# Optimization experiments

Hardware: AMD Instinct MI355X
Metric: run time of the kernel (lower is better)

Reference implementation:

```python
import jax, jax.numpy as jnp
import numpy as np

V = 32000   # vocab_size
D = 1024    # dim
NH = 16     # n_heads
HD = 64     # head_dim
L = 2       # n_layers
E = 8       # n_experts
K = 2       # n_active_experts
H = 2048    # expert_dim
B = 2
T = 1024
EPS = 1e-6
THETA = 10000.0
STD = 0.02


def rmsnorm(x, w):
    rms = jax.lax.rsqrt(jnp.mean(x * x, axis=-1, keepdims=True) + EPS)
    return x * rms * w


def rope_cos_sin(t_len):
    inv = 1.0 / (THETA ** (jnp.arange(0, HD, 2, dtype=jnp.float32) / HD))
    t = jnp.arange(t_len, dtype=jnp.float32)
    f = jnp.outer(t, inv)  # [T, HD//2]
    return jnp.cos(f), jnp.sin(f)


def apply_rope(x, cos, sin):
    # x: [B, T, NH, HD]; complex rotation on interleaved (even, odd) pairs
    xr = x[..., 0::2]
    xi = x[..., 1::2]
    c = cos[None, :, None, :]
    s = sin[None, :, None, :]
    out_r = xr * c - xi * s
    out_i = xr * s + xi * c
    return jnp.stack([out_r, out_i], axis=-1).reshape(x.shape)


def setup_inputs() -> dict:
    key = jax.random.key(0)
    ks = jax.random.split(key, 13)
    n = lambda k, shp: (jax.random.normal(k, shp, dtype=jnp.float32) * STD)
    return {
        "tokens": jax.random.randint(ks[0], (B, T), 0, V, dtype=jnp.int64)
                   if jax.config.jax_enable_x64 else
                   jax.random.randint(ks[0], (B, T), 0, V, dtype=jnp.int32),
        "emb": n(ks[1], (V, D)),            # tied embedding / output projection
        "attn_norm_w": jnp.ones((L, D), jnp.float32),
        "wq": n(ks[2], (L, D, D)),
        "wk": n(ks[3], (L, D, D)),
        "wv": n(ks[4], (L, D, D)),
        "wo": n(ks[5], (L, D, D)),
        "ffn_norm_w": jnp.ones((L, D), jnp.float32),
        "gate_w": n(ks[6], (L, D, E)),
        "w1": n(ks[7], (L, E, D, H)),
        "w2": n(ks[8], (L, E, H, D)),
        "w3": n(ks[9], (L, E, D, H)),
        "final_norm_w": jnp.ones((D,), jnp.float32),
    }


def reference(tokens, emb, attn_norm_w, wq, wk, wv, wo, ffn_norm_w,
              gate_w, w1, w2, w3, final_norm_w):
    b, t = tokens.shape
    h = emb[tokens]                                     # [B,T,D]
    cos, sin = rope_cos_sin(t)
    mask = jnp.where(jnp.tril(jnp.ones((t, t), bool)), 0.0, -jnp.inf)
    scale = 1.0 / np.sqrt(HD).astype(np.float32)
    aux_total = jnp.float32(0.0)

    for l in range(L):
        x = h
        # --- attention ---
        hn = rmsnorm(x, attn_norm_w[l])
        q = (hn @ wq[l]).reshape(b, t, NH, HD)
        k = (hn @ wk[l]).reshape(b, t, NH, HD)
        v = (hn @ wv[l]).reshape(b, t, NH, HD)
        q = apply_rope(q, cos, sin)
        k = apply_rope(k, cos, sin)
        scores = jnp.einsum('bqhd,bkhd->bhqk', q, k) * scale + mask
        attn = jax.nn.softmax(scores, axis=-1)
        o = jnp.einsum('bhqk,bkhd->bqhd', attn, v).reshape(b, t, D) @ wo[l]
        x = x + o
        # --- MoE ---
        xf = rmsnorm(x, ffn_norm_w[l]).reshape(-1, D)   # [N,D]
        gate_logits = xf @ gate_w[l]                    # [N,E]
        probs = jax.nn.softmax(gate_logits, axis=-1)
        vals, idx = jax.lax.top_k(probs, K)             # [N,K]
        w = vals / (jnp.sum(vals, axis=-1, keepdims=True) + 1e-8)
        oh = jax.nn.one_hot(idx, E, dtype=jnp.float32)  # [N,K,E]
        combine = jnp.sum(oh * w[..., None], axis=1)    # [N,E]
        tokens_per_expert = oh.sum(axis=1).mean(axis=0)
        aux_total = aux_total + E * jnp.sum(tokens_per_expert * probs.mean(axis=0))
        h1 = jnp.einsum('nd,edh->neh', xf, w1[l])
        h3 = jnp.einsum('nd,edh->neh', xf, w3[l])
        eo = jnp.einsum('neh,ehd->ned', jax.nn.silu(h1) * h3, w2[l])
        moe_out = jnp.einsum('ned,ne->nd', eo, combine).reshape(b, t, D)
        h = x + moe_out

    logits = rmsnorm(h, final_norm_w) @ emb.T           # [B,T,V]
    return logits, aux_total
```

## Files before the change

### kernel.cpp

```cpp
#include <hip/hip_runtime.h>
#include <hip/hip_bf16.h>
#include <math.h>

#define D_MODEL 1024
#define NHEADS  16
#define HDIM    64
#define NEXP    8
#define FFH     2048
#define BATCH   2
#define SEQ     1024
#define NTOK    2048
#define VOCAB   32000
#define LDSS    40

typedef __attribute__((ext_vector_type(4))) float f32x4;
typedef __attribute__((ext_vector_type(2))) float f32x2;
typedef __attribute__((ext_vector_type(8))) __bf16 bf16x8;
typedef __attribute__((ext_vector_type(4))) unsigned short u16x4;

__device__ __forceinline__ unsigned short f2bf(float f) {
    union { float f; unsigned u; } v; v.f = f;
    unsigned r = v.u + 0x7FFFu + ((v.u >> 16) & 1u);
    return (unsigned short)(r >> 16);
}
__device__ __forceinline__ float bf2f(unsigned short u) {
    union { unsigned u; float f; } v; v.u = ((unsigned)u) << 16; return v.f;
}
__device__ __forceinline__ void split3(float x, unsigned short& h, unsigned short& m, unsigned short& l) {
    h = f2bf(x);
    float r1 = x - bf2f(h);
    m = f2bf(r1);
    float r2 = r1 - bf2f(m);
    l = f2bf(r2);
}

#define MFMA(a, b, c) __builtin_amdgcn_mfma_f32_16x16x32_bf16((a), (b), (c), 0, 0, 0)

#define PSA ((long)NTOK * D_MODEL)
#define PSW ((long)D_MODEL * D_MODEL)

__global__ __launch_bounds__(256) void rmsnorm_kernel(const float* __restrict__ x,
    const float* __restrict__ wt, unsigned short* __restrict__ out3)
{
    __shared__ float red[4];
    int n = blockIdx.x;
    int c = threadIdx.x << 2;
    f32x4 v = *(const f32x4*)(x + (long)n*D_MODEL + c);
    float ss = v.x*v.x + v.y*v.y + v.z*v.z + v.w*v.w;
    #pragma unroll
    for (int dd = 32; dd; dd >>= 1) ss += __shfl_xor(ss, dd);
    if ((threadIdx.x & 63) == 0) red[threadIdx.x >> 6] = ss;
    __syncthreads();
    float tot = red[0] + red[1] + red[2] + red[3];
    float rms = rsqrtf(tot * (1.f / D_MODEL) + 1e-6f);
    f32x4 wv = *(const f32x4*)(wt + c);
    f32x4 o = v * rms;
    o = o * wv;
    u16x4 hv, mv, lv;
    #pragma unroll
    for (int j = 0; j < 4; j++) { unsigned short h,m,l; split3(o[j],h,m,l); hv[j]=h; mv[j]=m; lv[j]=l; }
    long idx = (long)n*D_MODEL + c;
    *(u16x4*)(out3 + 0*PSA + idx) = hv;
    *(u16x4*)(out3 + 1*PSA + idx) = mv;
    *(u16x4*)(out3 + 2*PSA + idx) = lv;
}

__global__ __launch_bounds__(256) void wsplitT_kernel(
    const float* __restrict__ wqs, const float* __restrict__ wks, const float* __restrict__ wvs,
    unsigned short* __restrict__ oq, unsigned short* __restrict__ ok, unsigned short* __restrict__ ov)
{
    __shared__ float t[64][65];
    int k0 = blockIdx.x*64, n0 = blockIdx.y*64, z = blockIdx.z;
    const float* src = (z==0) ? wqs : (z==1) ? wks : wvs;
    unsigned short* dst = (z==0) ? oq : (z==1) ? ok : ov;
    int tid = threadIdx.x;
    int a = tid & 63, g = tid >> 6;
    #pragma unroll 4
    for (int i = 0; i < 16; i++) {
        int k = g*16 + i;
        t[k][a] = src[(long)(k0+k)*D_MODEL + n0 + a];
    }
    __syncthreads();
    #pragma unroll 4
    for (int i = 0; i < 16; i++) {
        int n = g*16 + i;
        float v = t[a][n];
        unsigned short h,m,l; split3(v,h,m,l);
        long idx = (long)(n0+n)*D_MODEL + k0 + a;
        dst[0*PSW + idx] = h;
        dst[1*PSW + idx] = m;
        dst[2*PSW + idx] = l;
    }
}

__global__ __launch_bounds__(256, 4) void qkv_kernel(
    const unsigned short* __restrict__ A3,
    const unsigned short* __restrict__ Wq3, const unsigned short* __restrict__ Wk3,
    const unsigned short* __restrict__ Wv3,
    float* __restrict__ qf, float* __restrict__ kf, float* __restrict__ vf)
{
    __shared__ __align__(16) unsigned short As[3][64*LDSS];
    __shared__ __align__(16) unsigned short Bs[3][64*LDSS];
    int z = blockIdx.z;
    const unsigned short* B3 = (z==0) ? Wq3 : (z==1) ? Wk3 : Wv3;
    float* out = (z==0) ? qf : (z==1) ? kf : vf;
    int n0 = blockIdx.x*64, m0 = blockIdx.y*64;
    int tid = threadIdx.x, w = tid >> 6, lane = tid & 63;
    int wm = (w >> 1)*32, wn = (w & 1)*32;
    int lr = lane & 15, lg = lane >> 4;
    f32x4 zero = {0.f,0.f,0.f,0.f};
    f32x4 acc[2][2];
    #pragma unroll
    for (int mi = 0; mi < 2; mi++)
        #pragma unroll
        for (int ni = 0; ni < 2; ni++) acc[mi][ni] = zero;
    int rb = tid >> 3, kc = (tid & 7) << 2;

    for (int k0 = 0; k0 < D_MODEL; k0 += 32) {
        #pragma unroll
        for (int p = 0; p < 2; p++) {
            int r = p*32 + rb;
            #pragma unroll
            for (int s = 0; s < 3; s++) {
                *(u16x4*)&As[s][r*LDSS + kc] = *(const u16x4*)(A3 + s*PSA + (long)(m0+r)*D_MODEL + k0 + kc);
                *(u16x4*)&Bs[s][r*LDSS + kc] = *(const u16x4*)(B3 + s*PSW + (long)(n0+r)*D_MODEL + k0 + kc);
            }
        }
        __syncthreads();
        bf16x8 bf[3][2];
        #pragma unroll
        for (int s = 0; s < 3; s++)
            #pragma unroll
            for (int ni = 0; ni < 2; ni++)
                bf[s][ni] = *(const bf16x8*)&Bs[s][(wn + ni*16 + lr)*LDSS + lg*8];
        #pragma unroll
        for (int mi = 0; mi < 2; mi++) {
            bf16x8 ah = *(const bf16x8*)&As[0][(wm + mi*16 + lr)*LDSS + lg*8];
            bf16x8 am = *(const bf16x8*)&As[1][(wm + mi*16 + lr)*LDSS + lg*8];
            bf16x8 al = *(const bf16x8*)&As[2][(wm + mi*16 + lr)*LDSS + lg*8];
            #pragma unroll
            for (int ni = 0; ni < 2; ni++) {
                acc[mi][ni] = MFMA(ah, bf[0][ni], acc[mi][ni]);
                acc[mi][ni] = MFMA(ah, bf[1][ni], acc[mi][ni]);
                acc[mi][ni] = MFMA(am, bf[0][ni], acc[mi][ni]);
                acc[mi][ni] = MFMA(ah, bf[2][ni], acc[mi][ni]);
                acc[mi][ni] = MFMA(am, bf[1][ni], acc[mi][ni]);
                acc[mi][ni] = MFMA(al, bf[0][ni], acc[mi][ni]);
            }
        }
        __syncthreads();
    }
    #pragma unroll
    for (int mi = 0; mi < 2; mi++)
        #pragma unroll
        for (int r = 0; r < 4; r++) {
            long row = m0 + wm + mi*16 + lg*4 + r;
            #pragma unroll
            for (int ni = 0; ni < 2; ni++) {
                int col = n0 + wn + ni*16 + lr;
                out[row*D_MODEL + col] = acc[mi][ni][r];
            }
        }
}

__global__ __launch_bounds__(256, 3) void wo_kernel(
    const float* __restrict__ A, const float* __restrict__ B, float* h)
{
    __shared__ __align__(16) unsigned short As[3][64*LDSS];
    __shared__ __align__(16) unsigned short Bs[3][64*LDSS];
    int n0 = blockIdx.x*64, m0 = blockIdx.y*64;
    int tid = threadIdx.x, w = tid >> 6, lane = tid & 63;
    int wm = (w >> 1)*32, wn = (w & 1)*32;
    int lr = lane & 15, lg = lane >> 4;
    f32x4 zero = {0.f,0.f,0.f,0.f};
    f32x4 acc[2][2];
    #pragma unroll
    for (int mi = 0; mi < 2; mi++)
        #pragma unroll
        for (int ni = 0; ni < 2; ni++) acc[mi][ni] = zero;
    int rb = tid >> 3, kc = (tid & 7) << 2;
    int nb = (tid & 31) << 1, kb = (tid >> 5) << 2;

    for (int k0 = 0; k0 < D_MODEL; k0 += 32) {
        #pragma unroll
        for (int p = 0; p < 2; p++) {
            int r = p*32 + rb;
            f32x4 vv = *(const f32x4*)(A + (long)(m0+r)*D_MODEL + k0 + kc);
            u16x4 hv, mv, lv;
            #pragma unroll
            for (int j = 0; j < 4; j++) { unsigned short h,m,l; split3(vv[j],h,m,l); hv[j]=h; mv[j]=m; lv[j]=l; }
            *(u16x4*)&As[0][r*LDSS + kc] = hv;
            *(u16x4*)&As[1][r*LDSS + kc] = mv;
            *(u16x4*)&As[2][r*LDSS + kc] = lv;
        }
        {
            f32x2 c0 = *(const f32x2*)(B + (long)(k0+kb+0)*D_MODEL + n0 + nb);
            f32x2 c1 = *(const f32x2*)(B + (long)(k0+kb+1)*D_MODEL + n0 + nb);
            f32x2 c2 = *(const f32x2*)(B + (long)(k0+kb+2)*D_MODEL + n0 + nb);
            f32x2 c3 = *(const f32x2*)(B + (long)(k0+kb+3)*D_MODEL + n0 + nb);
            #pragma unroll
            for (int i = 0; i < 2; i++) {
                int r = nb + i;
                u16x4 hv, mv, lv;
                unsigned short h,m,l;
                split3(c0[i],h,m,l); hv[0]=h; mv[0]=m; lv[0]=l;
                split3(c1[i],h,m,l); hv[1]=h; mv[1]=m; lv[1]=l;
                split3(c2[i],h,m,l); hv[2]=h; mv[2]=m; lv[2]=l;
                split3(c3[i],h,m,l); hv[3]=h; mv[3]=m; lv[3]=l;
                *(u16x4*)&Bs[0][r*LDSS + kb] = hv;
                *(u16x4*)&Bs[1][r*LDSS + kb] = mv;
                *(u16x4*)&Bs[2][r*LDSS + kb] = lv;
            }
        }
        __syncthreads();
        bf16x8 bf[3][2];
        #pragma unroll
        for (int s = 0; s < 3; s++)
            #pragma unroll
            for (int ni = 0; ni < 2; ni++)
                bf[s][ni] = *(const bf16x8*)&Bs[s][(wn + ni*16 + lr)*LDSS + lg*8];
        #pragma unroll
        for (int mi = 0; mi < 2; mi++) {
            bf16x8 ah = *(const bf16x8*)&As[0][(wm + mi*16 + lr)*LDSS + lg*8];
            bf16x8 am = *(const bf16x8*)&As[1][(wm + mi*16 + lr)*LDSS + lg*8];
            bf16x8 al = *(const bf16x8*)&As[2][(wm + mi*16 + lr)*LDSS + lg*8];
            #pragma unroll
            for (int ni = 0; ni < 2; ni++) {
                acc[mi][ni] = MFMA(ah, bf[0][ni], acc[mi][ni]);
                acc[mi][ni] = MFMA(ah, bf[1][ni], acc[mi][ni]);
                acc[mi][ni] = MFMA(am, bf[0][ni], acc[mi][ni]);
                acc[mi][ni] = MFMA(ah, bf[2][ni], acc[mi][ni]);
                acc[mi][ni] = MFMA(am, bf[1][ni], acc[mi][ni]);
                acc[mi][ni] = MFMA(al, bf[0][ni], acc[mi][ni]);
            }
        }
        __syncthreads();
    }
    #pragma unroll
    for (int mi = 0; mi < 2; mi++)
        #pragma unroll
        for (int r = 0; r < 4; r++) {
            long row = m0 + wm + mi*16 + lg*4 + r;
            #pragma unroll
            for (int ni = 0; ni < 2; ni++) {
                int col = n0 + wn + ni*16 + lr;
                h[row*D_MODEL + col] += acc[mi][ni][r];
            }
        }
}

template<int SPLIT>
__global__ __launch_bounds__(256, 3) void moe13_kernel(
    const unsigned short* __restrict__ A3, const float* __restrict__ W1,
    const float* __restrict__ W3, float* __restrict__ G,
    const int* __restrict__ rowidx, const int* __restrict__ counts,
    const int* __restrict__ offsets)
{
    __shared__ __align__(16) unsigned short As[SPLIT][64*LDSS];
    __shared__ __align__(16) unsigned short Bs[SPLIT][128*LDSS];
    int e = blockIdx.z;
    int cnt = counts[e], off = offsets[e];
    int n0 = blockIdx.x*128, m0 = blockIdx.y*64;
    if (m0 >= cnt) return;
    const float* b1p = W1 + (long)e * (D_MODEL*FFH);
    const float* b3p = W3 + (long)e * (D_MODEL*FFH);
    int tid = threadIdx.x, w = tid >> 6, lane = tid & 63;
    int wm = (w >> 1)*32, wn = (w & 1)*64;
    int lr = lane & 15, lg = lane >> 4;
    f32x4 zero = {0.f,0.f,0.f,0.f};
    f32x4 a1[2][4], a3[2][4];
    #pragma unroll
    for (int mi = 0; mi < 2; mi++)
        #pragma unroll
        for (int ni = 0; ni < 4; ni++) { a1[mi][ni] = zero; a3[mi][ni] = zero; }
    int rb = tid >> 3, kc = (tid & 7) << 2;

    for (int k0 = 0; k0 < D_MODEL; k0 += 32) {
        #pragma unroll
        for (int p = 0; p < 2; p++) {
            int r = p*32 + rb;
            u16x4 z4 = {0,0,0,0};
            if (m0 + r < cnt) {
                long arow = (long)rowidx[off + m0 + r];
                #pragma unroll
                for (int s = 0; s < SPLIT; s++)
                    *(u16x4*)&As[s][r*LDSS + kc] = *(const u16x4*)(A3 + s*PSA + arow*D_MODEL + k0 + kc);
            } else {
                #pragma unroll
                for (int s = 0; s < SPLIT; s++)
                    *(u16x4*)&As[s][r*LDSS + kc] = z4;
            }
        }
        #pragma unroll
        for (int pass = 0; pass < 2; pass++) {
            const float* bp = pass ? b3p : b1p;
            f32x4 c0 = *(const f32x4*)(bp + (long)(k0+kc+0)*FFH + n0 + rb*4);
            f32x4 c1 = *(const f32x4*)(bp + (long)(k0+kc+1)*FFH + n0 + rb*4);
            f32x4 c2 = *(const f32x4*)(bp + (long)(k0+kc+2)*FFH + n0 + rb*4);
            f32x4 c3 = *(const f32x4*)(bp + (long)(k0+kc+3)*FFH + n0 + rb*4);
            #pragma unroll
            for (int i = 0; i < 4; i++) {
                int r = rb*4 + i;
                if (SPLIT == 3) {
                    u16x4 hv, mv, lv;
                    unsigned short h,m,l;
                    split3(c0[i],h,m,l); hv[0]=h; mv[0]=m; lv[0]=l;
                    split3(c1[i],h,m,l); hv[1]=h; mv[1]=m; lv[1]=l;
                    split3(c2[i],h,m,l); hv[2]=h; mv[2]=m; lv[2]=l;
                    split3(c3[i],h,m,l); hv[3]=h; mv[3]=m; lv[3]=l;
                    *(u16x4*)&Bs[0][r*LDSS + kc] = hv;
                    *(u16x4*)&Bs[1][r*LDSS + kc] = mv;
                    *(u16x4*)&Bs[2][r*LDSS + kc] = lv;
                } else {
                    u16x4 hv = {f2bf(c0[i]), f2bf(c1[i]), f2bf(c2[i]), f2bf(c3[i])};
                    *(u16x4*)&Bs[0][r*LDSS + kc] = hv;
                }
            }
            __syncthreads();
            bf16x8 bf[SPLIT][4];
            #pragma unroll
            for (int s = 0; s < SPLIT; s++)
                #pragma unroll
                for (int ni = 0; ni < 4; ni++)
                    bf[s][ni] = *(const bf16x8*)&Bs[s][(wn + ni*16 + lr)*LDSS + lg*8];
            #pragma unroll
            for (int mi = 0; mi < 2; mi++) {
                bf16x8 ah = *(const bf16x8*)&As[0][(wm + mi*16 + lr)*LDSS + lg*8];
                #pragma unroll
                for (int ni = 0; ni < 4; ni++) {
                    f32x4 a = pass ? a3[mi][ni] : a1[mi][ni];
                    a = MFMA(ah, bf[0][ni], a);
                    if (SPLIT == 3) {
                        bf16x8 am = *(const bf16x8*)&As[1][(wm + mi*16 + lr)*LDSS + lg*8];
                        bf16x8 al = *(const bf16x8*)&As[2][(wm + mi*16 + lr)*LDSS + lg*8];
                        a = MFMA(ah, bf[1][ni], a);
                        a = MFMA(am, bf[0][ni], a);
                        a = MFMA(ah, bf[2][ni], a);
                        a = MFMA(am, bf[1][ni], a);
                        a = MFMA(al, bf[0][ni], a);
                    }
                    if (pass) a3[mi][ni] = a; else a1[mi][ni] = a;
                }
            }
            __syncthreads();
        }
    }
    #pragma unroll
    for (int mi = 0; mi < 2; mi++)
        #pragma unroll
        for (int r = 0; r < 4; r++) {
            int rowl = wm + mi*16 + lg*4 + r;
            if (m0 + rowl < cnt) {
                long crow = off + m0 + rowl;
                #pragma unroll
                for (int ni = 0; ni < 4; ni++) {
                    int col = n0 + wn + ni*16 + lr;
                    float v1 = a1[mi][ni][r];
                    float v3 = a3[mi][ni][r];
                    G[crow*FFH + col] = (v1 / (1.f + expf(-v1))) * v3;
                }
            }
        }
}

template<int SPLIT>
__global__ __launch_bounds__(256, 4) void w2_kernel(
    const float* __restrict__ G, const float* __restrict__ W2, float* h,
    const int* __restrict__ rowidx, const float* __restrict__ wrow,
    const int* __restrict__ counts, const int* __restrict__ offsets)
{
    __shared__ __align__(16) unsigned short As[SPLIT][64*LDSS];
    __shared__ __align__(16) unsigned short Bs[SPLIT][64*LDSS];
    int e = blockIdx.z;
    int cnt = counts[e], off = offsets[e];
    int n0 = blockIdx.x*64, m0 = blockIdx.y*64;
    if (m0 >= cnt) return;
    const float* bp = W2 + (long)e * (FFH*D_MODEL);
    int tid = threadIdx.x, w = tid >> 6, lane = tid & 63;
    int wm = (w >> 1)*32, wn = (w & 1)*32;
    int lr = lane & 15, lg = lane >> 4;
    f32x4 zero = {0.f,0.f,0.f,0.f};
    f32x4 acc[2][2];
    #pragma unroll
    for (int mi = 0; mi < 2; mi++)
        #pragma unroll
        for (int ni = 0; ni < 2; ni++) acc[mi][ni] = zero;
    int rb = tid >> 3, kc = (tid & 7) << 2;
    int nb = (tid & 31) << 1, kb = (tid >> 5) << 2;

    for (int k0 = 0; k0 < FFH; k0 += 32) {
        #pragma unroll
        for (int p = 0; p < 2; p++) {
            int r = p*32 + rb;
            f32x4 vv = zero;
            if (m0 + r < cnt)
                vv = *(const f32x4*)(G + (long)(off + m0 + r)*FFH + k0 + kc);
            if (SPLIT == 3) {
                u16x4 hv, mv, lv;
                #pragma unroll
                for (int j = 0; j < 4; j++) { unsigned short h,m,l; split3(vv[j],h,m,l); hv[j]=h; mv[j]=m; lv[j]=l; }
                *(u16x4*)&As[0][r*LDSS + kc] = hv;
                *(u16x4*)&As[1][r*LDSS + kc] = mv;
                *(u16x4*)&As[2][r*LDSS + kc] = lv;
            } else {
                u16x4 hv;
                #pragma unroll
                for (int j = 0; j < 4; j++) hv[j] = f2bf(vv[j]);
                *(u16x4*)&As[0][r*LDSS + kc] = hv;
            }
        }
        {
            f32x2 c0 = *(const f32x2*)(bp + (long)(k0+kb+0)*D_MODEL + n0 + nb);
            f32x2 c1 = *(const f32x2*)(bp + (long)(k0+kb+1)*D_MODEL + n0 + nb);
            f32x2 c2 = *(const f32x2*)(bp + (long)(k0+kb+2)*D_MODEL + n0 + nb);
            f32x2 c3 = *(const f32x2*)(bp + (long)(k0+kb+3)*D_MODEL + n0 + nb);
            #pragma unroll
            for (int i = 0; i < 2; i++) {
                int r = nb + i;
                if (SPLIT == 3) {
                    u16x4 hv, mv, lv;
                    unsigned short h,m,l;
                    split3(c0[i],h,m,l); hv[0]=h; mv[0]=m; lv[0]=l;
                    split3(c1[i],h,m,l); hv[1]=h; mv[1]=m; lv[1]=l;
                    split3(c2[i],h,m,l); hv[2]=h; mv[2]=m; lv[2]=l;
                    split3(c3[i],h,m,l); hv[3]=h; mv[3]=m; lv[3]=l;
                    *(u16x4*)&Bs[0][r*LDSS + kb] = hv;
                    *(u16x4*)&Bs[1][r*LDSS + kb] = mv;
                    *(u16x4*)&Bs[2][r*LDSS + kb] = lv;
                } else {
                    u16x4 hv = {f2bf(c0[i]), f2bf(c1[i]), f2bf(c2[i]), f2bf(c3[i])};
                    *(u16x4*)&Bs[0][r*LDSS + kb] = hv;
                }
            }
        }
        __syncthreads();
        bf16x8 bf[SPLIT][2];
        #pragma unroll
        for (int s = 0; s < SPLIT; s++)
            #pragma unroll
            for (int ni = 0; ni < 2; ni++)
                bf[s][ni] = *(const bf16x8*)&Bs[s][(wn + ni*16 + lr)*LDSS + lg*8];
        #pragma unroll
        for (int mi = 0; mi < 2; mi++) {
            bf16x8 ah = *(const bf16x8*)&As[0][(wm + mi*16 + lr)*LDSS + lg*8];
            #pragma unroll
            for (int ni = 0; ni < 2; ni++) {
                acc[mi][ni] = MFMA(ah, bf[0][ni], acc[mi][ni]);
                if (SPLIT == 3) {
                    bf16x8 am = *(const bf16x8*)&As[1][(wm + mi*16 + lr)*LDSS + lg*8];
                    bf16x8 al = *(const bf16x8*)&As[2][(wm + mi*16 + lr)*LDSS + lg*8];
                    acc[mi][ni] = MFMA(ah, bf[1][ni], acc[mi][ni]);
                    acc[mi][ni] = MFMA(am, bf[0][ni], acc[mi][ni]);
                    acc[mi][ni] = MFMA(ah, bf[2][ni], acc[mi][ni]);
                    acc[mi][ni] = MFMA(am, bf[1][ni], acc[mi][ni]);
                    acc[mi][ni] = MFMA(al, bf[0][ni], acc[mi][ni]);
                }
            }
        }
        __syncthreads();
    }
    #pragma unroll
    for (int mi = 0; mi < 2; mi++)
        #pragma unroll
        for (int r = 0; r < 4; r++) {
            int rowl = wm + mi*16 + lg*4 + r;
            if (m0 + rowl < cnt) {
                long crow = off + m0 + rowl;
                long n = rowidx[crow];
                float wgt = wrow[crow];
                #pragma unroll
                for (int ni = 0; ni < 2; ni++) {
                    int col = n0 + wn + ni*16 + lr;
                    atomicAdd(&h[n*D_MODEL + col], wgt * acc[mi][ni][r]);
                }
            }
        }
}

__global__ __launch_bounds__(256) void attn_kernel(
    const float* __restrict__ q, const float* __restrict__ k,
    const float* __restrict__ v, float* __restrict__ att)
{
    __shared__ __align__(16) unsigned short Qs[3][64*72];
    __shared__ __align__(16) unsigned short KP[3][2560];
    __shared__ __align__(16) unsigned short Vt[3][2560];

    int qt = blockIdx.x, bh = blockIdx.y;
    int b = bh >> 4, hh = bh & 15;
    int tid = threadIdx.x, w = tid >> 6, lane = tid & 63;
    int lr = lane & 15, lg = lane >> 4;
    int lrow = tid >> 4;
    int lcol = (tid & 15) << 2;

    const float* qbase = q + ((long)(b*SEQ + qt*64) * D_MODEL + hh*64);
    #pragma unroll
    for (int p = 0; p < 4; p++) {
        int r = p*16 + lrow;
        f32x4 vv = *(const f32x4*)(qbase + (long)r * D_MODEL + lcol);
        #pragma unroll
        for (int jj = 0; jj < 4; jj++) {
            unsigned short h,m,l; split3(vv[jj],h,m,l);
            Qs[0][r*72 + lcol + jj] = h;
            Qs[1][r*72 + lcol + jj] = m;
            Qs[2][r*72 + lcol + jj] = l;
        }
    }

    f32x4 zero = {0.f,0.f,0.f,0.f};
    f32x4 oacc[4] = {zero, zero, zero, zero};
    float mrun[4] = {-INFINITY,-INFINITY,-INFINITY,-INFINITY};
    float lrun[4] = {0.f,0.f,0.f,0.f};

    int ntile = 2*qt + 2;
    for (int jt = 0; jt < ntile; jt++) {
        const float* kbase = k + ((long)(b*SEQ + jt*32) * D_MODEL + hh*64);
        const float* vbase = v + ((long)(b*SEQ + jt*32) * D_MODEL + hh*64);
        #pragma unroll
        for (int p = 0; p < 2; p++) {
            int r = p*16 + lrow;
            f32x4 kv4 = *(const f32x4*)(kbase + (long)r * D_MODEL + lcol);
            f32x4 vv4 = *(const f32x4*)(vbase + (long)r * D_MODEL + lcol);
            #pragma unroll
            for (int jj = 0; jj < 4; jj++) {
                unsigned short h,m,l;
                split3(kv4[jj],h,m,l);
                KP[0][r*72 + lcol + jj] = h;
                KP[1][r*72 + lcol + jj] = m;
                KP[2][r*72 + lcol + jj] = l;
                split3(vv4[jj],h,m,l);
                Vt[0][(lcol+jj)*40 + r] = h;
                Vt[1][(lcol+jj)*40 + r] = m;
                Vt[2][(lcol+jj)*40 + r] = l;
            }
        }
        __syncthreads();

        f32x4 s[2] = {zero, zero};
        #pragma unroll
        for (int ks = 0; ks < 2; ks++) {
            bf16x8 qh = *(const bf16x8*)&Qs[0][(w*16 + lr)*72 + ks*32 + lg*8];
            bf16x8 qm = *(const bf16x8*)&Qs[1][(w*16 + lr)*72 + ks*32 + lg*8];
            bf16x8 ql = *(const bf16x8*)&Qs[2][(w*16 + lr)*72 + ks*32 + lg*8];
            #pragma unroll
            for (int ni = 0; ni < 2; ni++) {
                bf16x8 kh = *(const bf16x8*)&KP[0][(ni*16 + lr)*72 + ks*32 + lg*8];
                bf16x8 km = *(const bf16x8*)&KP[1][(ni*16 + lr)*72 + ks*32 + lg*8];
                bf16x8 kl = *(const bf16x8*)&KP[2][(ni*16 + lr)*72 + ks*32 + lg*8];
                s[ni] = MFMA(qh, kh, s[ni]);
                s[ni] = MFMA(qh, km, s[ni]);
                s[ni] = MFMA(qm, kh, s[ni]);
                s[ni] = MFMA(qh, kl, s[ni]);
                s[ni] = MFMA(qm, km, s[ni]);
                s[ni] = MFMA(ql, kh, s[ni]);
            }
        }
        __syncthreads();

        #pragma unroll
        for (int r = 0; r < 4; r++) {
            int qg = qt*64 + w*16 + lg*4 + r;
            float mx = -INFINITY;
            #pragma unroll
            for (int ni = 0; ni < 2; ni++) {
                int kg = jt*32 + ni*16 + lr;
                float val = s[ni][r] * 0.125f;
                if (kg > qg) val = -INFINITY;
                s[ni][r] = val;
                mx = fmaxf(mx, val);
            }
            #pragma unroll
            for (int dd = 1; dd < 16; dd <<= 1)
                mx = fmaxf(mx, __shfl_xor(mx, dd));
            float mnew  = fmaxf(mrun[r], mx);
            float alpha = expf(mrun[r] - mnew);
            float ps = 0.f;
            #pragma unroll
            for (int ni = 0; ni < 2; ni++) {
                float pv = expf(s[ni][r] - mnew);
                s[ni][r] = pv;
                ps += pv;
            }
            #pragma unroll
            for (int dd = 1; dd < 16; dd <<= 1)
                ps += __shfl_xor(ps, dd);
            lrun[r] = lrun[r] * alpha + ps;
            mrun[r] = mnew;
            #pragma unroll
            for (int d = 0; d < 4; d++) oacc[d][r] *= alpha;
            int prow = w*16 + lg*4 + r;
            #pragma unroll
            for (int ni = 0; ni < 2; ni++) {
                unsigned short h,m,l; split3(s[ni][r],h,m,l);
                KP[0][prow*40 + ni*16 + lr] = h;
                KP[1][prow*40 + ni*16 + lr] = m;
                KP[2][prow*40 + ni*16 + lr] = l;
            }
        }
        {
            bf16x8 ph = *(const bf16x8*)&KP[0][(w*16 + lr)*40 + lg*8];
            bf16x8 pm = *(const bf16x8*)&KP[1][(w*16 + lr)*40 + lg*8];
            bf16x8 pl = *(const bf16x8*)&KP[2][(w*16 + lr)*40 + lg*8];
            #pragma unroll
            for (int ni = 0; ni < 4; ni++) {
                bf16x8 vh = *(const bf16x8*)&Vt[0][(ni*16 + lr)*40 + lg*8];
                bf16x8 vm = *(const bf16x8*)&Vt[1][(ni*16 + lr)*40 + lg*8];
                bf16x8 vl = *(const bf16x8*)&Vt[2][(ni*16 + lr)*40 + lg*8];
                oacc[ni] = MFMA(ph, vh, oacc[ni]);
                oacc[ni] = MFMA(ph, vm, oacc[ni]);
                oacc[ni] = MFMA(pm, vh, oacc[ni]);
                oacc[ni] = MFMA(ph, vl, oacc[ni]);
                oacc[ni] = MFMA(pm, vm, oacc[ni]);
                oacc[ni] = MFMA(pl, vh, oacc[ni]);
            }
        }
        __syncthreads();
    }
    float* obase = att + ((long)(b*SEQ + qt*64) * D_MODEL + hh*64);
    #pragma unroll
    for (int r = 0; r < 4; r++) {
        float inv = 1.f / lrun[r];
        #pragma unroll
        for (int ni = 0; ni < 4; ni++)
            obase[(long)(w*16 + lg*4 + r) * D_MODEL + ni*16 + lr] = oacc[ni][r] * inv;
    }
}

__global__ __launch_bounds__(256) void logits_kernel(
    const unsigned short* __restrict__ A0, const float* __restrict__ Bmat, float* __restrict__ C)
{
    __shared__ __align__(16) unsigned short As[128*LDSS];
    __shared__ __align__(16) unsigned short Bs[128*LDSS];
    int n0 = blockIdx.y * 128;
    int m0 = blockIdx.x * 128;
    int tid = threadIdx.x, w = tid >> 6, lane = tid & 63;
    int wm = (w >> 1)*64, wn = (w & 1)*64;
    int lr = lane & 15, lg = lane >> 4;
    f32x4 zero = {0.f,0.f,0.f,0.f};
    f32x4 acc[4][4];
    #pragma unroll
    for (int mi = 0; mi < 4; mi++)
        #pragma unroll
        for (int ni = 0; ni < 4; ni++) acc[mi][ni] = zero;
    int rb = tid >> 3, kc = (tid & 7) << 2;
    for (int k0 = 0; k0 < D_MODEL; k0 += 32) {
        #pragma unroll
        for (int p = 0; p < 4; p++) {
            int r = p*32 + rb;
            *(u16x4*)&As[r*LDSS + kc] = *(const u16x4*)(A0 + (long)(m0+r)*D_MODEL + k0 + kc);
            f32x4 vv = *(const f32x4*)(Bmat + (long)(n0+r)*D_MODEL + k0 + kc);
            u16x4 hv;
            #pragma unroll
            for (int j = 0; j < 4; j++) hv[j] = f2bf(vv[j]);
            *(u16x4*)&Bs[r*LDSS + kc] = hv;
        }
        __syncthreads();
        bf16x8 bfv[4], af[4];
        #pragma unroll
        for (int ni = 0; ni < 4; ni++)
            bfv[ni] = *(const bf16x8*)&Bs[(wn + ni*16 + lr)*LDSS + lg*8];
        #pragma unroll
        for (int mi = 0; mi < 4; mi++)
            af[mi] = *(const bf16x8*)&As[(wm + mi*16 + lr)*LDSS + lg*8];
        #pragma unroll
        for (int mi = 0; mi < 4; mi++)
            #pragma unroll
            for (int ni = 0; ni < 4; ni++)
                acc[mi][ni] = MFMA(af[mi], bfv[ni], acc[mi][ni]);
        __syncthreads();
    }
    #pragma unroll
    for (int mi = 0; mi < 4; mi++)
        #pragma unroll
        for (int r = 0; r < 4; r++) {
            long row = m0 + wm + mi*16 + lg*4 + r;
            #pragma unroll
            for (int ni = 0; ni < 4; ni++) {
                int col = n0 + wn + ni*16 + lr;
                C[row*VOCAB + col] = acc[mi][ni][r];
            }
        }
}

__global__ __launch_bounds__(256) void embed_kernel(const int* __restrict__ tok,
    const float* __restrict__ emb, float* __restrict__ h)
{
    int n = blockIdx.x;
    int c = threadIdx.x << 2;
    long t = tok[n];
    *(f32x4*)(h + (long)n*D_MODEL + c) = *(const f32x4*)(emb + t*D_MODEL + c);
}

__global__ __launch_bounds__(256) void ropetab_kernel(float* __restrict__ tab)
{
    int idx = blockIdx.x * 256 + threadIdx.x;
    if (idx >= SEQ * 32) return;
    int t = idx >> 5, i = idx & 31;
    double inv = pow(10000.0, -(double)(2*i) / 64.0);
    double ang = (double)t * inv;
    tab[idx*2]   = (float)cos(ang);
    tab[idx*2+1] = (float)sin(ang);
}

__global__ __launch_bounds__(256) void rope_kernel(float* __restrict__ q, float* __restrict__ kk,
    const float* __restrict__ tab)
{
    int gid = blockIdx.x * 256 + threadIdx.x;
    if (gid >= NTOK * 512) return;
    int n   = gid >> 9;
    int rem = gid & 511;
    int hh  = rem >> 5;
    int i   = rem & 31;
    int t   = n & (SEQ - 1);
    float cs = tab[(t*32 + i)*2];
    float sn = tab[(t*32 + i)*2 + 1];
    long base = (long)n * D_MODEL + hh*64 + 2*i;
    float qr = q[base], qi = q[base+1];
    q[base]   = qr*cs - qi*sn;
    q[base+1] = qr*sn + qi*cs;
    float kr = kk[base], ki = kk[base+1];
    kk[base]   = kr*cs - ki*sn;
    kk[base+1] = kr*sn + ki*cs;
}

__global__ __launch_bounds__(64) void gate_kernel(const unsigned short* __restrict__ xf3,
    const float* __restrict__ gw, int* __restrict__ counts,
    int* __restrict__ eid, float* __restrict__ wts, float* __restrict__ pbuf)
{
    int n = blockIdx.x;
    int lane = threadIdx.x;
    float acc[8] = {0,0,0,0,0,0,0,0};
    for (int d0 = lane*4; d0 < D_MODEL; d0 += 256) {
        long idx = (long)n*D_MODEL + d0;
        u16x4 xh = *(const u16x4*)(xf3 + 0*PSA + idx);
        u16x4 xm = *(const u16x4*)(xf3 + 1*PSA + idx);
        u16x4 xl = *(const u16x4*)(xf3 + 2*PSA + idx);
        #pragma unroll
        for (int j = 0; j < 4; j++) {
            float xv = bf2f(xh[j]) + bf2f(xm[j]) + bf2f(xl[j]);
            const float* g = gw + (d0+j) * 8;
            #pragma unroll
            for (int e = 0; e < 8; e++) acc[e] += xv * g[e];
        }
    }
    #pragma unroll
    for (int e = 0; e < 8; e++) {
        #pragma unroll
        for (int dd = 32; dd; dd >>= 1) acc[e] += __shfl_xor(acc[e], dd);
    }
    if (lane == 0) {
        float mx = acc[0];
        #pragma unroll
        for (int e = 1; e < 8; e++) mx = fmaxf(mx, acc[e]);
        float pe[8], ssum = 0.f;
        #pragma unroll
        for (int e = 0; e < 8; e++) { pe[e] = expf(acc[e] - mx); ssum += pe[e]; }
        float sinv = 1.f / ssum;
        #pragma unroll
        for (int e = 0; e < 8; e++) { pe[e] *= sinv; pbuf[n*8 + e] = pe[e]; }
        int e1 = 0;
        #pragma unroll
        for (int e = 1; e < 8; e++) if (pe[e] > pe[e1]) e1 = e;
        int e2 = -1;
        #pragma unroll
        for (int e = 0; e < 8; e++) if (e != e1 && (e2 < 0 || pe[e] > pe[e2])) e2 = e;
        float v1 = pe[e1], v2 = pe[e2];
        float wsum = v1 + v2 + 1e-8f;
        eid[n*2] = e1; eid[n*2+1] = e2;
        wts[n*2] = v1 / wsum; wts[n*2+1] = v2 / wsum;
        atomicAdd(counts + e1, 1);
        atomicAdd(counts + e2, 1);
    }
}

__global__ __launch_bounds__(64) void scan_kernel(const int* __restrict__ counts,
    int* __restrict__ offs, int* __restrict__ cursor,
    const float* __restrict__ pbuf, float* __restrict__ aux)
{
    int t = threadIdx.x;
    int e = t & 7, c = t >> 3;
    float s = 0.f;
    for (int n = 0; n < NTOK/8; n++)
        s += pbuf[(c*(NTOK/8) + n)*8 + e];
    #pragma unroll
    for (int dd = 8; dd < 64; dd <<= 1) s += __shfl_xor(s, dd);
    __shared__ float red[8];
    if (t < 8) red[t] = s;
    __syncthreads();
    if (t == 0) {
        int o = 0; float a = 0.f;
        for (int k = 0; k < 8; k++) {
            offs[k] = o; cursor[k] = o; o += counts[k];
            a += (float)counts[k] * red[k];
        }
        aux[0] += 8.f * a / ((float)NTOK * (float)NTOK);
    }
}

__global__ __launch_bounds__(256) void assign_kernel(const int* __restrict__ eid,
    const float* __restrict__ wts, int* __restrict__ cursor,
    int* __restrict__ rowidx, float* __restrict__ wrow)
{
    int n = blockIdx.x * 256 + threadIdx.x;
    if (n >= NTOK) return;
    #pragma unroll
    for (int s = 0; s < 2; s++) {
        int e = eid[n*2 + s];
        int p = atomicAdd(cursor + e, 1);
        rowidx[p] = n;
        wrow[p] = wts[n*2 + s];
    }
}

__global__ void write_aux_kernel(float* __restrict__ out, const float* __restrict__ aux)
{
    if (threadIdx.x == 0 && blockIdx.x == 0)
        out[(long)NTOK * VOCAB] = aux[0];
}

extern "C" void kernel_launch(void* const* d_in, const int* in_sizes, int n_in,
                              void* d_out, int out_size, void* d_ws, size_t ws_size,
                              hipStream_t stream)
{
    const int*   tokens = (const int*)d_in[0];
    const float* emb    = (const float*)d_in[1];
    const float* anw    = (const float*)d_in[2];
    const float* wq     = (const float*)d_in[3];
    const float* wk     = (const float*)d_in[4];
    const float* wv     = (const float*)d_in[5];
    const float* wo     = (const float*)d_in[6];
    const float* fnw    = (const float*)d_in[7];
    const float* gw     = (const float*)d_in[8];
    const float* w1     = (const float*)d_in[9];
    const float* w2     = (const float*)d_in[10];
    const float* w3     = (const float*)d_in[11];
    const float* finw   = (const float*)d_in[12];
    float* out = (float*)d_out;

    char* W = (char*)d_ws;
    const size_t MB = 1024u * 1024u;
    int*   counts = (int*)(W + 0);
    int*   offs   = (int*)(W + 64);
    int*   cursor = (int*)(W + 128);
    float* aux    = (float*)(W + 192);
    int*   eid    = (int*)(W + 4096);
    float* wts    = (float*)(W + 4096 + 16384);
    int*   rowix  = (int*)(W + 4096 + 32768);
    float* wrow   = (float*)(W + 4096 + 49152);
    float* pbuf   = (float*)(W + 4096 + 65536);
    float* rtab   = (float*)(W + 4096 + 131072 + 65536);
    float*          h    = (float*)(W + 1*MB);
    unsigned short* hn3  = (unsigned short*)(W + 9*MB);
    float*          qf   = (float*)(W + 21*MB);
    float*          kf   = (float*)(W + 29*MB);
    float*          vf   = (float*)(W + 37*MB);
    unsigned short* wq3  = (unsigned short*)(W + 45*MB);
    unsigned short* wk3  = (unsigned short*)(W + 51*MB);
    unsigned short* wv3  = (unsigned short*)(W + 57*MB);
    float*          att  = (float*)(W + 45*MB);
    float*          g    = (float*)(W + 21*MB);

    hipMemsetAsync(W, 0, 256, stream);
    ropetab_kernel<<<(SEQ*32 + 255)/256, 256, 0, stream>>>(rtab);
    embed_kernel<<<NTOK, 256, 0, stream>>>(tokens, emb, h);

    for (int l = 0; l < 2; l++) {
        const float* wql = wq + (size_t)l*D_MODEL*D_MODEL;
        const float* wkl = wk + (size_t)l*D_MODEL*D_MODEL;
        const float* wvl = wv + (size_t)l*D_MODEL*D_MODEL;
        const float* wol = wo + (size_t)l*D_MODEL*D_MODEL;

        rmsnorm_kernel<<<NTOK, 256, 0, stream>>>(h, anw + (size_t)l*D_MODEL, hn3);
        wsplitT_kernel<<<dim3(16, 16, 3), 256, 0, stream>>>(wql, wkl, wvl, wq3, wk3, wv3);
        qkv_kernel<<<dim3(D_MODEL/64, NTOK/64, 3), 256, 0, stream>>>(hn3, wq3, wk3, wv3, qf, kf, vf);
        rope_kernel<<<(NTOK*512 + 255)/256, 256, 0, stream>>>(qf, kf, rtab);
        attn_kernel<<<dim3(SEQ/64, BATCH*NHEADS), 256, 0, stream>>>(qf, kf, vf, att);
        wo_kernel<<<dim3(D_MODEL/64, NTOK/64), 256, 0, stream>>>(att, wol, h);

        rmsnorm_kernel<<<NTOK, 256, 0, stream>>>(h, fnw + (size_t)l*D_MODEL, hn3);
        hipMemsetAsync(W, 0, 160, stream);
        gate_kernel<<<NTOK, 64, 0, stream>>>(hn3, gw + (size_t)l*D_MODEL*NEXP, counts, eid, wts, pbuf);
        scan_kernel<<<1, 64, 0, stream>>>(counts, offs, cursor, pbuf, aux);
        assign_kernel<<<(NTOK + 255)/256, 256, 0, stream>>>(eid, wts, cursor, rowix, wrow);

        const float* w1l = w1 + (size_t)l*NEXP*D_MODEL*FFH;
        const float* w3l = w3 + (size_t)l*NEXP*D_MODEL*FFH;
        const float* w2l = w2 + (size_t)l*NEXP*FFH*D_MODEL;
        dim3 g13(FFH/128, 2*NTOK/64, NEXP);
        dim3 g2d(D_MODEL/64, 2*NTOK/64, NEXP);
        if (l == 0) {
            moe13_kernel<3><<<g13, 256, 0, stream>>>(hn3, w1l, w3l, g, rowix, counts, offs);
            w2_kernel<3><<<g2d, 256, 0, stream>>>(g, w2l, h, rowix, wrow, counts, offs);
        } else {
            moe13_kernel<1><<<g13, 256, 0, stream>>>(hn3, w1l, w3l, g, rowix, counts, offs);
            w2_kernel<1><<<g2d, 256, 0, stream>>>(g, w2l, h, rowix, wrow, counts, offs);
        }
    }

    rmsnorm_kernel<<<NTOK, 256, 0, stream>>>(h, finw, hn3);
    logits_kernel<<<dim3(NTOK/128, VOCAB/128), 256, 0, stream>>>(hn3, emb, out);
    write_aux_kernel<<<1, 1, 0, stream>>>(out, aux);
}
```

Measured before the change: 2.056 ms.

## Register-prefetch next K-tile in GEMM kernels and use truncating bf16 split

Adds register double-buffering to the wo, expert up-projection and down-projection GEMMs: global loads for the next K tile are issued before the barrier and MFMA work of the current tile, so memory latency overlaps with compute. The w1/w3 pass loop is unrolled into two explicit phases, each with its own prefetched operand. It also adds a split3t that takes the high and mid bf16 parts by truncation rather than round-to-nearest, and uses it in place of split3 in these GEMMs and in attention. The prefetch raises register pressure, which may lower occupancy, and truncation changes the rounding of the three-way split.

```diff
diff --git a/kernel.cpp b/kernel.cpp
--- a/kernel.cpp
+++ b/kernel.cpp
@@ -30,6 +30,15 @@
     h = f2bf(x);
     float r1 = x - bf2f(h);
     m = f2bf(r1);
+    float r2 = r1 - bf2f(m);
+    l = f2bf(r2);
+}
+__device__ __forceinline__ void split3t(float x, unsigned short& h, unsigned short& m, unsigned short& l) {
+    union { float f; unsigned u; } a; a.f = x;
+    h = (unsigned short)(a.u >> 16);
+    float r1 = x - bf2f(h);
+    union { float f; unsigned u; } b; b.f = r1;
+    m = (unsigned short)(b.u >> 16);
     float r2 = r1 - bf2f(m);
     l = f2bf(r2);
 }
@@ -181,36 +190,47 @@
     int rb = tid >> 3, kc = (tid & 7) << 2;
     int nb = (tid & 31) << 1, kb = (tid >> 5) << 2;
 
+    f32x4 pAv[2];
+    f32x2 pBv[4];
+    #pragma unroll
+    for (int p = 0; p < 2; p++)
+        pAv[p] = *(const f32x4*)(A + (long)(m0 + p*32 + rb)*D_MODEL + kc);
+    #pragma unroll
+    for (int i = 0; i < 4; i++)
+        pBv[i] = *(const f32x2*)(B + (long)(kb + i)*D_MODEL + n0 + nb);
+
     for (int k0 = 0; k0 < D_MODEL; k0 += 32) {
+        int kn = k0 + 32;
         #pragma unroll
         for (int p = 0; p < 2; p++) {
             int r = p*32 + rb;
-            f32x4 vv = *(const f32x4*)(A + (long)(m0+r)*D_MODEL + k0 + kc);
             u16x4 hv, mv, lv;
             #pragma unroll
-            for (int j = 0; j < 4; j++) { unsigned short h,m,l; split3(vv[j],h,m,l); hv[j]=h; mv[j]=m; lv[j]=l; }
+            for (int j = 0; j < 4; j++) { unsigned short h,m,l; split3t(pAv[p][j],h,m,l); hv[j]=h; mv[j]=m; lv[j]=l; }
             *(u16x4*)&As[0][r*LDSS + kc] = hv;
             *(u16x4*)&As[1][r*LDSS + kc] = mv;
             *(u16x4*)&As[2][r*LDSS + kc] = lv;
         }
-        {
-            f32x2 c0 = *(const f32x2*)(B + (long)(k0+kb+0)*D_MODEL + n0 + nb);
-            f32x2 c1 = *(const f32x2*)(B + (long)(k0+kb+1)*D_MODEL + n0 + nb);
-            f32x2 c2 = *(const f32x2*)(B + (long)(k0+kb+2)*D_MODEL + n0 + nb);
-            f32x2 c3 = *(const f32x2*)(B + (long)(k0+kb+3)*D_MODEL + n0 + nb);
-            #pragma unroll
-            for (int i = 0; i < 2; i++) {
-                int r = nb + i;
-                u16x4 hv, mv, lv;
-                unsigned short h,m,l;
-                split3(c0[i],h,m,l); hv[0]=h; mv[0]=m; lv[0]=l;
-                split3(c1[i],h,m,l); hv[1]=h; mv[1]=m; lv[1]=l;
-                split3(c2[i],h,m,l); hv[2]=h; mv[2]=m; lv[2]=l;
-                split3(c3[i],h,m,l); hv[3]=h; mv[3]=m; lv[3]=l;
-                *(u16x4*)&Bs[0][r*LDSS + kb] = hv;
-                *(u16x4*)&Bs[1][r*LDSS + kb] = mv;
-                *(u16x4*)&Bs[2][r*LDSS + kb] = lv;
-            }
+        #pragma unroll
+        for (int i = 0; i < 2; i++) {
+            int r = nb + i;
+            u16x4 hv, mv, lv;
+            unsigned short h,m,l;
+            split3t(pBv[0][i],h,m,l); hv[0]=h; mv[0]=m; lv[0]=l;
+            split3t(pBv[1][i],h,m,l); hv[1]=h; mv[1]=m; lv[1]=l;
+            split3t(pBv[2][i],h,m,l); hv[2]=h; mv[2]=m; lv[2]=l;
+            split3t(pBv[3][i],h,m,l); hv[3]=h; mv[3]=m; lv[3]=l;
+            *(u16x4*)&Bs[0][r*LDSS + kb] = hv;
+            *(u16x4*)&Bs[1][r*LDSS + kb] = mv;
+            *(u16x4*)&Bs[2][r*LDSS + kb] = lv;
+        }
+        if (kn < D_MODEL) {
+            #pragma unroll
+            for (int p = 0; p < 2; p++)
+                pAv[p] = *(const f32x4*)(A + (long)(m0 + p*32 + rb)*D_MODEL + kn + kc);
+            #pragma unroll
+            for (int i = 0; i < 4; i++)
+                pBv[i] = *(const f32x2*)(B + (long)(kn + kb + i)*D_MODEL + n0 + nb);
         }
         __syncthreads();
         bf16x8 bf[3][2];
@@ -275,48 +295,64 @@
         for (int ni = 0; ni < 4; ni++) { a1[mi][ni] = zero; a3[mi][ni] = zero; }
     int rb = tid >> 3, kc = (tid & 7) << 2;
 
+    long arow[2]; int av[2];
+    #pragma unroll
+    for (int p = 0; p < 2; p++) {
+        int r = p*32 + rb;
+        av[p] = (m0 + r < cnt) ? 1 : 0;
+        arow[p] = av[p] ? (long)rowidx[off + m0 + r] : 0;
+    }
+    u16x4 z4 = {0,0,0,0};
+    u16x4 pA[2][SPLIT];
+    f32x4 p1[4], p3[4];
+    #pragma unroll
+    for (int p = 0; p < 2; p++)
+        #pragma unroll
+        for (int s = 0; s < SPLIT; s++)
+            pA[p][s] = av[p] ? *(const u16x4*)(A3 + s*PSA + arow[p]*D_MODEL + kc) : z4;
+    #pragma unroll
+    for (int i = 0; i < 4; i++) {
+        p1[i] = *(const f32x4*)(b1p + (long)(kc + i)*FFH + n0 + rb*4);
+        p3[i] = *(const f32x4*)(b3p + (long)(kc + i)*FFH + n0 + rb*4);
+    }
+
     for (int k0 = 0; k0 < D_MODEL; k0 += 32) {
-        #pragma unroll
-        for (int p = 0; p < 2; p++) {
-            int r = p*32 + rb;
-            u16x4 z4 = {0,0,0,0};
-            if (m0 + r < cnt) {
-                long arow = (long)rowidx[off + m0 + r];
+        int kn = k0 + 32;
+        #pragma unroll
+        for (int p = 0; p < 2; p++)
+            #pragma unroll
+            for (int s = 0; s < SPLIT; s++)
+                *(u16x4*)&As[s][(p*32 + rb)*LDSS + kc] = pA[p][s];
+        #pragma unroll
+        for (int i = 0; i < 4; i++) {
+            int r = rb*4 + i;
+            if (SPLIT == 3) {
+                u16x4 hv, mv, lv;
+                unsigned short h,m,l;
+                split3t(p1[0][i],h,m,l); hv[0]=h; mv[0]=m; lv[0]=l;
+                split3t(p1[1][i],h,m,l); hv[1]=h; mv[1]=m; lv[1]=l;
+                split3t(p1[2][i],h,m,l); hv[2]=h; mv[2]=m; lv[2]=l;
+                split3t(p1[3][i],h,m,l); hv[3]=h; mv[3]=m; lv[3]=l;
+                *(u16x4*)&Bs[0][r*LDSS + kc] = hv;
+                *(u16x4*)&Bs[1][r*LDSS + kc] = mv;
+                *(u16x4*)&Bs[2][r*LDSS + kc] = lv;
+            } else {
+                u16x4 hv = {f2bf(p1[0][i]), f2bf(p1[1][i]), f2bf(p1[2][i]), f2bf(p1[3][i])};
+                *(u16x4*)&Bs[0][r*LDSS + kc] = hv;
+            }
+        }
+        if (kn < D_MODEL) {
+            #pragma unroll
+            for (int p = 0; p < 2; p++)
                 #pragma unroll
                 for (int s = 0; s < SPLIT; s++)
-                    *(u16x4*)&As[s][r*LDSS + kc] = *(const u16x4*)(A3 + s*PSA + arow*D_MODEL + k0 + kc);
-            } else {
-                #pragma unroll
-                for (int s = 0; s < SPLIT; s++)
-                    *(u16x4*)&As[s][r*LDSS + kc] = z4;
-            }
-        }
-        #pragma unroll
-        for (int pass = 0; pass < 2; pass++) {
-            const float* bp = pass ? b3p : b1p;
-            f32x4 c0 = *(const f32x4*)(bp + (long)(k0+kc+0)*FFH + n0 + rb*4);
-            f32x4 c1 = *(const f32x4*)(bp + (long)(k0+kc+1)*FFH + n0 + rb*4);
-            f32x4 c2 = *(const f32x4*)(bp + (long)(k0+kc+2)*FFH + n0 + rb*4);
-            f32x4 c3 = *(const f32x4*)(bp + (long)(k0+kc+3)*FFH + n0 + rb*4);
-            #pragma unroll
-            for (int i = 0; i < 4; i++) {
-                int r = rb*4 + i;
-                if (SPLIT == 3) {
-                    u16x4 hv, mv, lv;
-                    unsigned short h,m,l;
-                    split3(c0[i],h,m,l); hv[0]=h; mv[0]=m; lv[0]=l;
-                    split3(c1[i],h,m,l); hv[1]=h; mv[1]=m; lv[1]=l;
-                    split3(c2[i],h,m,l); hv[2]=h; mv[2]=m; lv[2]=l;
-                    split3(c3[i],h,m,l); hv[3]=h; mv[3]=m; lv[3]=l;
-                    *(u16x4*)&Bs[0][r*LDSS + kc] = hv;
-                    *(u16x4*)&Bs[1][r*LDSS + kc] = mv;
-                    *(u16x4*)&Bs[2][r*LDSS + kc] = lv;
-                } else {
-                    u16x4 hv = {f2bf(c0[i]), f2bf(c1[i]), f2bf(c2[i]), f2bf(c3[i])};
-                    *(u16x4*)&Bs[0][r*LDSS + kc] = hv;
-                }
-            }
-            __syncthreads();
+                    pA[p][s] = av[p] ? *(const u16x4*)(A3 + s*PSA + arow[p]*D_MODEL + kn + kc) : z4;
+            #pragma unroll
+            for (int i = 0; i < 4; i++)
+                p1[i] = *(const f32x4*)(b1p + (long)(kn + kc + i)*FFH + n0 + rb*4);
+        }
+        __syncthreads();
+        {
             bf16x8 bf[SPLIT][4];
             #pragma unroll
             for (int s = 0; s < SPLIT; s++)
@@ -328,7 +364,7 @@
                 bf16x8 ah = *(const bf16x8*)&As[0][(wm + mi*16 + lr)*LDSS + lg*8];
                 #pragma unroll
                 for (int ni = 0; ni < 4; ni++) {
-                    f32x4 a = pass ? a3[mi][ni] : a1[mi][ni];
+                    f32x4 a = a1[mi][ni];
                     a = MFMA(ah, bf[0][ni], a);
                     if (SPLIT == 3) {
                         bf16x8 am = *(const bf16x8*)&As[1][(wm + mi*16 + lr)*LDSS + lg*8];
@@ -339,11 +375,63 @@
                         a = MFMA(am, bf[1][ni], a);
                         a = MFMA(al, bf[0][ni], a);
                     }
-                    if (pass) a3[mi][ni] = a; else a1[mi][ni] = a;
+                    a1[mi][ni] = a;
                 }
             }
-            __syncthreads();
-        }
+        }
+        __syncthreads();
+        #pragma unroll
+        for (int i = 0; i < 4; i++) {
+            int r = rb*4 + i;
+            if (SPLIT == 3) {
+                u16x4 hv, mv, lv;
+                unsigned short h,m,l;
+                split3t(p3[0][i],h,m,l); hv[0]=h; mv[0]=m; lv[0]=l;
+                split3t(p3[1][i],h,m,l); hv[1]=h; mv[1]=m; lv[1]=l;
+                split3t(p3[2][i],h,m,l); hv[2]=h; mv[2]=m; lv[2]=l;
+                split3t(p3[3][i],h,m,l); hv[3]=h; mv[3]=m; lv[3]=l;
+                *(u16x4*)&Bs[0][r*LDSS + kc] = hv;
+                *(u16x4*)&Bs[1][r*LDSS + kc] = mv;
+                *(u16x4*)&Bs[2][r*LDSS + kc] = lv;
+            } else {
+                u16x4 hv = {f2bf(p3[0][i]), f2bf(p3[1][i]), f2bf(p3[2][i]), f2bf(p3[3][i])};
+                *(u16x4*)&Bs[0][r*LDSS + kc] = hv;
+            }
+        }
+        if (kn < D_MODEL) {
+            #pragma unroll
+            for (int i = 0; i < 4; i++)
+                p3[i] = *(const f32x4*)(b3p + (long)(kn + kc + i)*FFH + n0 + rb*4);
+        }
+        __syncthreads();
+        {
+            bf16x8 bf[SPLIT][4];
+            #pragma unroll
+            for (int s = 0; s < SPLIT; s++)
+                #pragma unroll
+                for (int ni = 0; ni < 4; ni++)
+                    bf[s][ni] = *(const bf16x8*)&Bs[s][(wn + ni*16 + lr)*LDSS + lg*8];
+            #pragma unroll
+            for (int mi = 0; mi < 2; mi++) {
+                bf16x8 ah = *(const bf16x8*)&As[0][(wm + mi*16 + lr)*LDSS + lg*8];
+                #pragma unroll
+                for (int ni = 0; ni < 4; ni++) {
+                    f32x4 a = a3[mi][ni];
+                    a = MFMA(ah, bf[0][ni], a);
+                    if (SPLIT == 3) {
+                        bf16x8 am = *(const bf16x8*)&As[1][(wm + mi*16 + lr)*LDSS + lg*8];
+                        bf16x8 al = *(const bf16x8*)&As[2][(wm + mi*16 + lr)*LDSS + lg*8];
+                        a = MFMA(ah, bf[1][ni], a);
+                        a = MFMA(am, bf[0][ni], a);
+                        a = MFMA(ah, bf[2][ni], a);
+                        a = MFMA(am, bf[1][ni], a);
+                        a = MFMA(al, bf[0][ni], a);
+                    }
+                    a3[mi][ni] = a;
+                }
+            }
+        }
+        __syncthreads();
     }
     #pragma unroll
     for (int mi = 0; mi < 2; mi++)
@@ -388,50 +476,62 @@
     int rb = tid >> 3, kc = (tid & 7) << 2;
     int nb = (tid & 31) << 1, kb = (tid >> 5) << 2;
 
+    int av[2];
+    #pragma unroll
+    for (int p = 0; p < 2; p++) av[p] = (m0 + p*32 + rb < cnt) ? 1 : 0;
+    f32x4 pG[2];
+    f32x2 pW[4];
+    #pragma unroll
+    for (int p = 0; p < 2; p++)
+        pG[p] = av[p] ? *(const f32x4*)(G + (long)(off + m0 + p*32 + rb)*FFH + kc) : zero;
+    #pragma unroll
+    for (int i = 0; i < 4; i++)
+        pW[i] = *(const f32x2*)(bp + (long)(kb + i)*D_MODEL + n0 + nb);
+
     for (int k0 = 0; k0 < FFH; k0 += 32) {
+        int kn = k0 + 32;
         #pragma unroll
         for (int p = 0; p < 2; p++) {
             int r = p*32 + rb;
-            f32x4 vv = zero;
-            if (m0 + r < cnt)
-                vv = *(const f32x4*)(G + (long)(off + m0 + r)*FFH + k0 + kc);
             if (SPLIT == 3) {
                 u16x4 hv, mv, lv;
                 #pragma unroll
-                for (int j = 0; j < 4; j++) { unsigned short h,m,l; split3(vv[j],h,m,l); hv[j]=h; mv[j]=m; lv[j]=l; }
+                for (int j = 0; j < 4; j++) { unsigned short h,m,l; split3t(pG[p][j],h,m,l); hv[j]=h; mv[j]=m; lv[j]=l; }
                 *(u16x4*)&As[0][r*LDSS + kc] = hv;
                 *(u16x4*)&As[1][r*LDSS + kc] = mv;
                 *(u16x4*)&As[2][r*LDSS + kc] = lv;
             } else {
                 u16x4 hv;
                 #pragma unroll
-                for (int j = 0; j < 4; j++) hv[j] = f2bf(vv[j]);
+                for (int j = 0; j < 4; j++) hv[j] = f2bf(pG[p][j]);
                 *(u16x4*)&As[0][r*LDSS + kc] = hv;
             }
         }
-        {
-            f32x2 c0 = *(const f32x2*)(bp + (long)(k0+kb+0)*D_MODEL + n0 + nb);
-            f32x2 c1 = *(const f32x2*)(bp + (long)(k0+kb+1)*D_MODEL + n0 + nb);
-            f32x2 c2 = *(const f32x2*)(bp + (long)(k0+kb+2)*D_MODEL + n0 + nb);
-            f32x2 c3 = *(const f32x2*)(bp + (long)(k0+kb+3)*D_MODEL + n0 + nb);
-            #pragma unroll
-            for (int i = 0; i < 2; i++) {
-                int r = nb + i;
-                if (SPLIT == 3) {
-                    u16x4 hv, mv, lv;
-                    unsigned short h,m,l;
-                    split3(c0[i],h,m,l); hv[0]=h; mv[0]=m; lv[0]=l;
-                    split3(c1[i],h,m,l); hv[1]=h; mv[1]=m; lv[1]=l;
-                    split3(c2[i],h,m,l); hv[2]=h; mv[2]=m; lv[2]=l;
-                    split3(c3[i],h,m,l); hv[3]=h; mv[3]=m; lv[3]=l;
-                    *(u16x4*)&Bs[0][r*LDSS + kb] = hv;
-                    *(u16x4*)&Bs[1][r*LDSS + kb] = mv;
-                    *(u16x4*)&Bs[2][r*LDSS + kb] = lv;
-                } else {
-                    u16x4 hv = {f2bf(c0[i]), f2bf(c1[i]), f2bf(c2[i]), f2bf(c3[i])};
-                    *(u16x4*)&Bs[0][r*LDSS + kb] = hv;
-                }
-            }
+        #pragma unroll
+        for (int i = 0; i < 2; i++) {
+            int r = nb + i;
+            if (SPLIT == 3) {
+                u16x4 hv, mv, lv;
+                unsigned short h,m,l;
+                split3t(pW[0][i],h,m,l); hv[0]=h; mv[0]=m; lv[0]=l;
+                split3t(pW[1][i],h,m,l); hv[1]=h; mv[1]=m; lv[1]=l;
+                split3t(pW[2][i],h,m,l); hv[2]=h; mv[2]=m; lv[2]=l;
+                split3t(pW[3][i],h,m,l); hv[3]=h; mv[3]=m; lv[3]=l;
+                *(u16x4*)&Bs[0][r*LDSS + kb] = hv;
+                *(u16x4*)&Bs[1][r*LDSS + kb] = mv;
+                *(u16x4*)&Bs[2][r*LDSS + kb] = lv;
+            } else {
+                u16x4 hv = {f2bf(pW[0][i]), f2bf(pW[1][i]), f2bf(pW[2][i]), f2bf(pW[3][i])};
+                *(u16x4*)&Bs[0][r*LDSS + kb] = hv;
+            }
+        }
+        if (kn < FFH) {
+            #pragma unroll
+            for (int p = 0; p < 2; p++)
+                pG[p] = av[p] ? *(const f32x4*)(G + (long)(off + m0 + p*32 + rb)*FFH + kn + kc) : zero;
+            #pragma unroll
+            for (int i = 0; i < 4; i++)
+                pW[i] = *(const f32x2*)(bp + (long)(kn + kb + i)*D_MODEL + n0 + nb);
         }
         __syncthreads();
         bf16x8 bf[SPLIT][2];
@@ -499,7 +599,7 @@
         f32x4 vv = *(const f32x4*)(qbase + (long)r * D_MODEL + lcol);
         #pragma unroll
         for (int jj = 0; jj < 4; jj++) {
-            unsigned short h,m,l; split3(vv[jj],h,m,l);
+            unsigned short h,m,l; split3t(vv[jj],h,m,l);
             Qs[0][r*72 + lcol + jj] = h;
             Qs[1][r*72 + lcol + jj] = m;
             Qs[2][r*72 + lcol + jj] = l;
@@ -523,11 +623,11 @@
             #pragma unroll
             for (int jj = 0; jj < 4; jj++) {
                 unsigned short h,m,l;
-                split3(kv4[jj],h,m,l);
+                split3t(kv4[jj],h,m,l);
                 KP[0][r*72 + lcol + jj] = h;
                 KP[1][r*72 + lcol + jj] = m;
                 KP[2][r*72 + lcol + jj] = l;
-                split3(vv4[jj],h,m,l);
+                split3t(vv4[jj],h,m,l);
                 Vt[0][(lcol+jj)*40 + r] = h;
                 Vt[1][(lcol+jj)*40 + r] = m;
                 Vt[2][(lcol+jj)*40 + r] = l;
@@ -590,7 +690,7 @@
             int prow = w*16 + lg*4 + r;
             #pragma unroll
             for (int ni = 0; ni < 2; ni++) {
-                unsigned short h,m,l; split3(s[ni][r],h,m,l);
+                unsigned short h,m,l; split3t(s[ni][r],h,m,l);
                 KP[0][prow*40 + ni*16 + lr] = h;
                 KP[1][prow*40 + ni*16 + lr] = m;
                 KP[2][prow*40 + ni*16 + lr] = l;
```

Measured after the change: 2.097 ms. 2.0% more time.
